# Kernel optimization log

Hardware: AMD Instinct MI355X
Metric: run time of the kernel (lower is better)

The kernel has to match this reference:

```python
import jax, jax.numpy as jnp
import numpy as np

TEMP = 5.0  # temperature_init
# All C(4,2)=6 keep-2-of-4 patterns for 2:4 semi-structured sparsity
PATTERNS = jnp.array([[1,1,0,0],[1,0,1,0],[1,0,0,1],[0,1,1,0],[0,1,0,1],[0,0,1,1]], dtype=jnp.float32)


def masked_linear(x, w, b, alpha, ids):
    # x: [N, I], w: [O, I], alpha: [A, O, I//4, 6], ids: [N]
    A, O, G, P = alpha.shape
    probs = jax.nn.softmax(alpha / TEMP, axis=-1)            # [A, O, G, 6]
    mask = jnp.einsum('aogp,pk->aogk', probs, PATTERNS)      # [A, O, G, 4]
    wm = w[None, :, :] * mask.reshape(A, O, G * 4)           # [A, O, I] per-agent masked weight
    y = jnp.einsum('ni,aoi->nao', x, wm)                     # dense per-agent GEMM
    y = jnp.take_along_axis(y, ids[:, None, None], axis=1)[:, 0, :]
    return y + b


def gru_cell(x, h, w_ih, w_hh, b_ih, b_hh):
    gi = x @ w_ih.T + b_ih
    gh = h @ w_hh.T + b_hh
    i_r, i_z, i_n = jnp.split(gi, 3, axis=-1)
    h_r, h_z, h_n = jnp.split(gh, 3, axis=-1)
    r = jax.nn.sigmoid(i_r + h_r)
    z = jax.nn.sigmoid(i_z + h_z)
    n = jnp.tanh(i_n + r * h_n)
    return (1.0 - z) * n + z * h


def setup_inputs() -> dict:
    key = jax.random.key(0)
    ks = jax.random.split(key, 20)
    B, A, E, H, NA = 1024, 8, 64, 512, 16
    s = 0.05
    d = {}
    d['inputs'] = jax.random.normal(ks[0], (B, A, E), jnp.float32)
    d['hidden_state'] = jax.random.normal(ks[1], (B, A, H), jnp.float32)
    d['agent_ids'] = jax.random.randint(ks[2], (B, A), 0, A, jnp.int32)
    d['fc1_w'] = jax.random.normal(ks[3], (H, E), jnp.float32) * s
    d['fc1_b'] = jax.random.normal(ks[4], (H,), jnp.float32) * s
    d['fc1_alpha'] = jax.random.normal(ks[5], (A, H, E // 4, 6), jnp.float32)
    d['gru_w_ih'] = jax.random.normal(ks[6], (3 * H, H), jnp.float32) * s
    d['gru_w_hh'] = jax.random.normal(ks[7], (3 * H, H), jnp.float32) * s
    d['gru_b_ih'] = jax.random.normal(ks[8], (3 * H,), jnp.float32) * s
    d['gru_b_hh'] = jax.random.normal(ks[9], (3 * H,), jnp.float32) * s
    d['fc2_w'] = jax.random.normal(ks[10], (H, H), jnp.float32) * s
    d['fc2_b'] = jax.random.normal(ks[11], (H,), jnp.float32) * s
    d['fc2_alpha'] = jax.random.normal(ks[12], (A, H, H // 4, 6), jnp.float32)
    d['fc3_w'] = jax.random.normal(ks[13], (H, H), jnp.float32) * s
    d['fc3_b'] = jax.random.normal(ks[14], (H,), jnp.float32) * s
    d['fc3_alpha'] = jax.random.normal(ks[15], (A, H, H // 4, 6), jnp.float32)
    d['fc4_w'] = jax.random.normal(ks[16], (NA, H), jnp.float32) * s
    d['fc4_b'] = jax.random.normal(ks[17], (NA,), jnp.float32) * s
    d['fc4_alpha'] = jax.random.normal(ks[18], (A, NA, H // 4, 6), jnp.float32)
    return d


def reference(inputs, hidden_state, agent_ids,
              fc1_w, fc1_b, fc1_alpha,
              gru_w_ih, gru_w_hh, gru_b_ih, gru_b_hh,
              fc2_w, fc2_b, fc2_alpha,
              fc3_w, fc3_b, fc3_alpha,
              fc4_w, fc4_b, fc4_alpha):
    b, a, e = inputs.shape
    H = hidden_state.shape[-1]
    x = inputs.reshape(-1, e)
    ids = agent_ids.reshape(-1)
    x = jax.nn.relu(masked_linear(x, fc1_w, fc1_b, fc1_alpha, ids))
    h = gru_cell(x, hidden_state.reshape(-1, H), gru_w_ih, gru_w_hh, gru_b_ih, gru_b_hh)
    q = jax.nn.relu(masked_linear(h, fc2_w, fc2_b, fc2_alpha, ids))
    q = jax.nn.relu(masked_linear(q, fc3_w, fc3_b, fc3_alpha, ids))
    q = masked_linear(q, fc4_w, fc4_b, fc4_alpha, ids)
    return q.reshape(b, a, -1), h.reshape(b, a, -1)
```

## Files before the change

kernel.cpp:

```cpp
#include <hip/hip_runtime.h>
#include <hip/hip_bf16.h>

typedef unsigned short ushort_t;
typedef __bf16 bf16x8 __attribute__((ext_vector_type(8)));
typedef unsigned short us8 __attribute__((ext_vector_type(8)));
typedef float f32x4 __attribute__((ext_vector_type(4)));

__device__ __forceinline__ ushort_t f2b(float f) {
    union { float f; unsigned int u; } v; v.f = f;
    unsigned int u = v.u;
    unsigned int r = (u + 0x7FFFu + ((u >> 16) & 1u)) >> 16;
    return (ushort_t)r;
}
__device__ __forceinline__ float sigmoidf_(float x) {
    return 1.f / (1.f + __expf(-x));
}
__device__ __forceinline__ void store_o(ushort_t* p, float v) { *p = f2b(v); }
__device__ __forceinline__ void store_o(float* p, float v) { *p = v; }

__global__ void fill_kernel(float* out, long long n, float val) {
    long long i = (long long)blockIdx.x * blockDim.x + threadIdx.x;
    if (i < n) out[i] = val;
}

#define PACKSZ(O, K) ((long long)((O) >= 64 ? (O) >> 6 : 1) * ((K) >> 5) * 2048)

__device__ __forceinline__ void maskw_item(const float* __restrict__ alpha,
                                           const float* __restrict__ w,
                                           ushort_t* __restrict__ wm,
                                           long long idx, int O, int G, int dup) {
    int g = (int)(idx % G);
    long long t2 = idx / G;
    int o = (int)(t2 % O);
    int a = (int)(t2 / O);
    const float* al = alpha + idx * 6;
    float p[6];
    float mx = -1e30f;
    #pragma unroll
    for (int i = 0; i < 6; i++) { p[i] = al[i] * 0.2f; mx = fmaxf(mx, p[i]); }
    float s = 0.f;
    #pragma unroll
    for (int i = 0; i < 6; i++) { p[i] = __expf(p[i] - mx); s += p[i]; }
    float inv = 1.f / s;
    #pragma unroll
    for (int i = 0; i < 6; i++) p[i] *= inv;
    float mk[4] = { p[0] + p[1] + p[2], p[0] + p[3] + p[4],
                    p[1] + p[3] + p[5], p[2] + p[4] + p[5] };
    int K = G * 4;
    const float* wr = w + (long long)o * K + g * 4;
    ushort_t* base = wm + (long long)a * PACKSZ(O, K);
    int k0 = g * 4;
    int c = o >> 6, su = (o >> 4) & 3, n = o & 15;
    int kk = k0 >> 5, q = (k0 >> 3) & 3, e0 = k0 & 7;
    long long off = (((long long)(c * (K >> 5) + kk) * 4 + su) * 64 + (q * 16 + n)) * 8 + e0;
    #pragma unroll
    for (int t = 0; t < 4; t++) {
        ushort_t v = f2b(wr[t] * mk[t]);
        base[off + t] = v;
        if (dup) {
            base[off + t + 512] = v;
            base[off + t + 1024] = v;
            base[off + t + 1536] = v;
        }
    }
}

__device__ __forceinline__ void canon_pack_item(const float* __restrict__ src,
                                                ushort_t* __restrict__ dst,
                                                long long i) {
    long long base = i * 8;
    int o_full = (int)(base >> 9);
    int k0 = (int)(base & 511);
    int g = o_full >> 9, o = o_full & 511;
    int c = o >> 6, su = (o >> 4) & 3, n = o & 15;
    int kk = k0 >> 5, q = (k0 >> 3) & 3;
    long long off = (long long)g * 262144 +
        (((long long)(c * 16 + kk) * 4 + su) * 64 + (q * 16 + n)) * 8;
    us8 v;
    #pragma unroll
    for (int e = 0; e < 8; e++) v[e] = f2b(src[base + e]);
    *(us8*)(dst + off) = v;
}

__device__ __forceinline__ void canon_gather_item(const float* __restrict__ src,
                                                  ushort_t* __restrict__ dst,
                                                  const int* __restrict__ perm,
                                                  int ld, long long i) {
    long long base = i * 8;
    int pos = (int)(base / ld);
    int k = (int)(base % ld);
    int row = perm[pos] & 8191;
    const float* s = src + (long long)row * ld + k;
    us8 v;
    #pragma unroll
    for (int e = 0; e < 8; e++) v[e] = f2b(s[e]);
    *(us8*)(dst + base) = v;
}

#define W_FC1 65536LL
#define W_FC2 589824LL
#define W_FC3 1114112LL
#define W_FC4 1130496LL
#define W_WIH 1228800LL
#define W_END 1327104LL
#define SPW_BLOCKS (1 + 1296)

__global__ void sort_prepw(const int* __restrict__ ids,
                           int* __restrict__ perm, int* __restrict__ seg,
                           int4* __restrict__ ttab, int* __restrict__ tcount,
                           const float* fc1_al, const float* fc1_w, ushort_t* wm1,
                           const float* fc2_al, const float* fc2_w, ushort_t* wm2,
                           const float* fc3_al, const float* fc3_w, ushort_t* wm3,
                           const float* fc4_al, const float* fc4_w, ushort_t* wm4,
                           const float* wih, ushort_t* wihp,
                           const float* whh, ushort_t* whhp) {
    int tid = threadIdx.x;
    if (blockIdx.x == 0) {
        __shared__ int hist[16][8];
        __shared__ int wbase[16][8];
        __shared__ int atot[8];
        __shared__ int abase[8];
        int wave = tid >> 6, lane = tid & 63;
        int base = wave * 512;
        unsigned long long lt = (lane == 63) ? 0x7fffffffffffffffull
                                             : ((1ull << lane) - 1ull);
        int myid[8], rank[8];
        int run[8] = {0, 0, 0, 0, 0, 0, 0, 0};
        #pragma unroll
        for (int i = 0; i < 8; i++) myid[i] = ids[base + i * 64 + lane] & 7;
        #pragma unroll
        for (int i = 0; i < 8; i++) {
            int a = myid[i];
            int r = 0;
            #pragma unroll
            for (int a2 = 0; a2 < 8; a2++) {
                unsigned long long m = __ballot(a == a2);
                if (a2 == a) r = run[a2] + __popcll(m & lt);
                run[a2] += __popcll(m);
            }
            rank[i] = r;
        }
        if (lane == 0) {
            #pragma unroll
            for (int a = 0; a < 8; a++) hist[wave][a] = run[a];
        }
        __syncthreads();
        if (tid < 8) {
            int a = tid, s = 0;
            for (int w = 0; w < 16; w++) { wbase[w][a] = s; s += hist[w][a]; }
            atot[a] = s;
        }
        __syncthreads();
        if (tid == 0) {
            int s = 0;
            for (int a = 0; a < 8; a++) { abase[a] = s; seg[a] = s; s += atot[a]; }
            seg[8] = s;
            int T = 0;
            for (int a = 0; a < 8; a++)
                for (int m = abase[a]; m < abase[a] + atot[a]; m += 64) {
                    int e = abase[a] + atot[a];
                    if (e > m + 64) e = m + 64;
                    ttab[T++] = make_int4(a, m, e, 0);
                }
            *tcount = T;
        }
        __syncthreads();
        #pragma unroll
        for (int i = 0; i < 8; i++) {
            int a = myid[i];
            perm[abase[a] + wbase[wave][a] + rank[i]] = base + i * 64 + lane;
        }
        return;
    }
    long long gid = (long long)(blockIdx.x - 1) * 1024 + tid;
    if (gid < W_FC1)      { maskw_item(fc1_al, fc1_w, wm1, gid, 512, 16, 0); return; }
    if (gid < W_FC2)      { maskw_item(fc2_al, fc2_w, wm2, gid - W_FC1, 512, 128, 0); return; }
    if (gid < W_FC3)      { maskw_item(fc3_al, fc3_w, wm3, gid - W_FC2, 512, 128, 0); return; }
    if (gid < W_FC4)      { maskw_item(fc4_al, fc4_w, wm4, gid - W_FC3, 16, 128, 1); return; }
    if (gid < W_WIH)      { canon_pack_item(wih, wihp, gid - W_FC4); return; }
    canon_pack_item(whh, whhp, gid - W_WIH);
}

#define G_INP 65536LL
#define G_END 589824LL
#define PG_BLOCKS 576

__global__ void prep_gather(const float* __restrict__ inputs, ushort_t* inp_pos,
                            const float* __restrict__ hidden, ushort_t* hid_pos,
                            const int* __restrict__ perm) {
    long long gid = (long long)blockIdx.x * 1024 + threadIdx.x;
    if (gid < G_INP) canon_gather_item(inputs, inp_pos, perm, 64, gid);
    else             canon_gather_item(hidden, hid_pos, perm, 512, gid - G_INP);
}

#define BM 64
#define BN 64

template <typename OT>
__launch_bounds__(256, 4)
__global__ void gemm_tiled(const ushort_t* __restrict__ In, int ldin,
                           const ushort_t* __restrict__ Wpk, long long wstride,
                           const float* __restrict__ bias,
                           OT* __restrict__ Out, int ldo,
                           const int4* __restrict__ ttab,
                           const int* __restrict__ tcount,
                           const int* __restrict__ scatter,
                           int O, int K, int relu) {
    int t = blockIdx.x;
    if (t >= *tcount) return;
    int4 tt = ttab[t];
    int a = tt.x, pos0 = tt.y, pos1 = tt.z;
    int o0 = blockIdx.y * BN;

    __shared__ ushort_t As[2][2048];

    int tid = threadIdx.x;
    int wave = tid >> 6, lane = tid & 63;
    int wr = (wave >> 1) & 1, wc = wave & 1;
    int quad = lane >> 4, l16 = lane & 15;
    int srow = tid >> 2, sgrp = tid & 3;
    int wsoff = (srow * 4 + (sgrp ^ ((srow >> 2) & 3))) * 8;
    int rl = (l16 * 4 + (quad ^ ((l16 >> 2) & 3))) * 8;

    int apos = pos0 + srow;
    int apos_c = apos < pos1 ? apos : (pos1 - 1);
    const ushort_t* aptr = In + (long long)apos_c * ldin + sgrp * 8;

    const ushort_t* wb = Wpk + (long long)a * wstride +
        (long long)blockIdx.y * (K >> 5) * 2048 + lane * 8;

    f32x4 acc[2][2];
    #pragma unroll
    for (int i = 0; i < 2; i++)
        #pragma unroll
        for (int j = 0; j < 2; j++) acc[i][j] = (f32x4){0.f, 0.f, 0.f, 0.f};

    int KKh = K >> 6;
    for (int k2 = 0; k2 < KKh; k2++) {
        int kk = k2 * 2;
        us8 av0 = *(const us8*)(aptr + kk * 32);
        us8 av1 = *(const us8*)(aptr + kk * 32 + 32);
        bf16x8 b00 = *(const bf16x8*)(wb + (kk * 4 + wc * 2 + 0) * 512);
        bf16x8 b01 = *(const bf16x8*)(wb + (kk * 4 + wc * 2 + 1) * 512);
        bf16x8 b10 = *(const bf16x8*)(wb + ((kk + 1) * 4 + wc * 2 + 0) * 512);
        bf16x8 b11 = *(const bf16x8*)(wb + ((kk + 1) * 4 + wc * 2 + 1) * 512);
        __syncthreads();
        *(us8*)(&As[0][wsoff]) = av0;
        *(us8*)(&As[1][wsoff]) = av1;
        __syncthreads();
        bf16x8 af0[2], af1[2];
        af0[0] = *(const bf16x8*)(&As[0][(wr * 2 + 0) * 512 + rl]);
        af0[1] = *(const bf16x8*)(&As[0][(wr * 2 + 1) * 512 + rl]);
        af1[0] = *(const bf16x8*)(&As[1][(wr * 2 + 0) * 512 + rl]);
        af1[1] = *(const bf16x8*)(&As[1][(wr * 2 + 1) * 512 + rl]);
        #pragma unroll
        for (int i = 0; i < 2; i++) {
            acc[i][0] = __builtin_amdgcn_mfma_f32_16x16x32_bf16(af0[i], b00, acc[i][0], 0, 0, 0);
            acc[i][1] = __builtin_amdgcn_mfma_f32_16x16x32_bf16(af0[i], b01, acc[i][1], 0, 0, 0);
        }
        #pragma unroll
        for (int i = 0; i < 2; i++) {
            acc[i][0] = __builtin_amdgcn_mfma_f32_16x16x32_bf16(af1[i], b10, acc[i][0], 0, 0, 0);
            acc[i][1] = __builtin_amdgcn_mfma_f32_16x16x32_bf16(af1[i], b11, acc[i][1], 0, 0, 0);
        }
    }

    #pragma unroll
    for (int i = 0; i < 2; i++) {
        int mbase = wr * 32 + i * 16 + quad * 4;
        #pragma unroll
        for (int j = 0; j < 2; j++) {
            int col = o0 + wc * 32 + j * 16 + l16;
            if (col < O) {
                float bias_v = bias ? bias[col] : 0.f;
                #pragma unroll
                for (int r = 0; r < 4; r++) {
                    int pos = pos0 + mbase + r;
                    if (pos < pos1) {
                        float v = acc[i][j][r] + bias_v;
                        if (relu) v = fmaxf(v, 0.f);
                        int orow = (scatter ? scatter[pos] : pos) & 8191;
                        store_o(&Out[(long long)orow * ldo + col], v);
                    }
                }
            }
        }
    }
}

__launch_bounds__(512, 2)
__global__ void gru_fused(const ushort_t* __restrict__ y1,
                          const ushort_t* __restrict__ hid_pos,
                          const float* __restrict__ hidden_f,
                          const ushort_t* __restrict__ wihp,
                          const ushort_t* __restrict__ whhp,
                          const float* __restrict__ bih,
                          const float* __restrict__ bhh,
                          const int* __restrict__ perm,
                          float* __restrict__ out_h_f,
                          ushort_t* __restrict__ hp,
                          int N, int H) {
    int m0 = blockIdx.x * 128;

    __shared__ ushort_t Ay[4096];
    __shared__ ushort_t Ah[4096];
    __shared__ ushort_t Bt[6][2048];

    int tid = threadIdx.x;
    int wave = tid >> 6, lane = tid & 63;
    int wr = wave >> 1, wc = wave & 1;
    int quad = lane >> 4, l16 = lane & 15;
    int srow = tid >> 2, sgrp = tid & 3;
    int wsoff = (srow * 4 + (sgrp ^ ((srow >> 2) & 3))) * 8;
    int rl = (l16 * 4 + (quad ^ ((l16 >> 2) & 3))) * 8;

    const ushort_t* ay_p = y1 + (long long)(m0 + srow) * H + sgrp * 8;
    const ushort_t* ah_p = hid_pos + (long long)(m0 + srow) * H + sgrp * 8;

    const ushort_t* wbs[3];
    int wg[3];
    #pragma unroll
    for (int q = 0; q < 3; q++) {
        int s = q * 512 + tid;
        int g = s >> 8, so = s & 255;
        wg[q] = s;
        wbs[q] = ((g < 3) ? (wihp + (long long)g * 262144)
                          : (whhp + (long long)(g - 3) * 262144)) +
                 (long long)blockIdx.y * 16 * 2048 + so * 8;
    }

    f32x4 acc[4][2][2];
    #pragma unroll
    for (int g = 0; g < 4; g++)
        #pragma unroll
        for (int i = 0; i < 2; i++)
            #pragma unroll
            for (int j = 0; j < 2; j++) acc[g][i][j] = (f32x4){0.f, 0.f, 0.f, 0.f};

    for (int kk = 0; kk < 16; kk++) {
        us8 va = *(const us8*)(ay_p + kk * 32);
        us8 vh = *(const us8*)(ah_p + kk * 32);
        us8 vb[3];
        #pragma unroll
        for (int q = 0; q < 3; q++) vb[q] = *(const us8*)(wbs[q] + kk * 2048);
        __syncthreads();
        *(us8*)(&Ay[wsoff]) = va;
        *(us8*)(&Ah[wsoff]) = vh;
        #pragma unroll
        for (int q = 0; q < 3; q++) {
            int s = wg[q];
            *(us8*)(&Bt[s >> 8][(s & 255) * 8]) = vb[q];
        }
        __syncthreads();

        bf16x8 ayf[2], ahf[2];
        #pragma unroll
        for (int u = 0; u < 2; u++) {
            ayf[u] = *(const bf16x8*)(&Ay[(wr * 2 + u) * 512 + rl]);
            ahf[u] = *(const bf16x8*)(&Ah[(wr * 2 + u) * 512 + rl]);
        }
        #pragma unroll
        for (int g = 0; g < 3; g++) {
            bf16x8 bw[2], bu[2];
            #pragma unroll
            for (int u = 0; u < 2; u++) {
                bw[u] = *(const bf16x8*)(&Bt[g][(wc * 2 + u) * 512 + lane * 8]);
                bu[u] = *(const bf16x8*)(&Bt[g + 3][(wc * 2 + u) * 512 + lane * 8]);
            }
            int ai = (g < 2) ? g : 2;
            int ah2 = (g < 2) ? g : 3;
            #pragma unroll
            for (int i = 0; i < 2; i++)
                #pragma unroll
                for (int j = 0; j < 2; j++) {
                    acc[ai][i][j] = __builtin_amdgcn_mfma_f32_16x16x32_bf16(
                        ayf[i], bw[j], acc[ai][i][j], 0, 0, 0);
                    acc[ah2][i][j] = __builtin_amdgcn_mfma_f32_16x16x32_bf16(
                        ahf[i], bu[j], acc[ah2][i][j], 0, 0, 0);
                }
        }
    }

    int c0 = blockIdx.y * 64;
    #pragma unroll
    for (int i = 0; i < 2; i++) {
        #pragma unroll
        for (int r = 0; r < 4; r++) {
            int pos = m0 + wr * 32 + i * 16 + quad * 4 + r;
            int norig = perm[pos] & 8191;
            #pragma unroll
            for (int j = 0; j < 2; j++) {
                int col = c0 + wc * 32 + j * 16 + l16;
                float sr = acc[0][i][j][r] + bih[col] + bhh[col];
                float sz = acc[1][i][j][r] + bih[H + col] + bhh[H + col];
                float in_ = acc[2][i][j][r] + bih[2 * H + col];
                float hn = acc[3][i][j][r] + bhh[2 * H + col];
                float rg = sigmoidf_(sr);
                float zg = sigmoidf_(sz);
                float ng = tanhf(in_ + rg * hn);
                float hv = hidden_f[(long long)norig * H + col];
                float hnew = (1.f - zg) * ng + zg * hv;
                out_h_f[(long long)norig * H + col] = hnew;
                hp[(long long)pos * H + col] = f2b(hnew);
            }
        }
    }
}

extern "C" void kernel_launch(void* const* d_in, const int* in_sizes, int n_in,
                              void* d_out, int out_size, void* d_ws, size_t ws_size,
                              hipStream_t stream) {
    (void)in_sizes; (void)n_in;
    const int N = 8192, A = 8, E = 64, H = 512, NA = 16;

    float* out_f = (float*)d_out;
    float* out_q = out_f;
    float* out_h = out_f + (size_t)N * NA;

    char* p = (char*)d_ws;
    auto alloc = [&](size_t b) { char* r = p; p += (b + 255) & ~(size_t)255; return r; };
    int*  perm   = (int*)alloc((size_t)N * 4);
    int*  seg    = (int*)alloc(16 * 4);
    int4* ttab   = (int4*)alloc(144 * 16);
    int*  tcount = (int*)alloc(256);
    ushort_t* wm1     = (ushort_t*)alloc((size_t)A * PACKSZ(H, E) * 2);
    ushort_t* wm2     = (ushort_t*)alloc((size_t)A * PACKSZ(H, H) * 2);
    ushort_t* wm3     = (ushort_t*)alloc((size_t)A * PACKSZ(H, H) * 2);
    ushort_t* wm4     = (ushort_t*)alloc((size_t)A * PACKSZ(NA, H) * 2);
    ushort_t* y1      = (ushort_t*)alloc((size_t)N * H * 2);
    ushort_t* inp_pos = (ushort_t*)alloc((size_t)N * E * 2);
    ushort_t* hid_pos = (ushort_t*)alloc((size_t)N * H * 2);
    ushort_t* wihp    = (ushort_t*)alloc((size_t)3 * H * H * 2);
    ushort_t* whhp    = (ushort_t*)alloc((size_t)3 * H * H * 2);
    ushort_t* hp      = (ushort_t*)alloc((size_t)N * H * 2);
    size_t need = (size_t)(p - (char*)d_ws);
    ushort_t* q2 = y1;
    ushort_t* q3 = hid_pos;

    if (ws_size < need) {
        fill_kernel<<<(unsigned)((out_size + 255) / 256), 256, 0, stream>>>(
            out_f, out_size, 1000.f);
        return;
    }

    const float* inputs = (const float*)d_in[0];
    const float* hidden = (const float*)d_in[1];
    const int*   ids    = (const int*)d_in[2];
    const float* fc1_w  = (const float*)d_in[3];
    const float* fc1_b  = (const float*)d_in[4];
    const float* fc1_al = (const float*)d_in[5];
    const float* wih    = (const float*)d_in[6];
    const float* whh    = (const float*)d_in[7];
    const float* bih    = (const float*)d_in[8];
    const float* bhh    = (const float*)d_in[9];
    const float* fc2_w  = (const float*)d_in[10];
    const float* fc2_b  = (const float*)d_in[11];
    const float* fc2_al = (const float*)d_in[12];
    const float* fc3_w  = (const float*)d_in[13];
    const float* fc3_b  = (const float*)d_in[14];
    const float* fc3_al = (const float*)d_in[15];
    const float* fc4_w  = (const float*)d_in[16];
    const float* fc4_b  = (const float*)d_in[17];
    const float* fc4_al = (const float*)d_in[18];

    sort_prepw<<<SPW_BLOCKS, 1024, 0, stream>>>(
        ids, perm, seg, ttab, tcount,
        fc1_al, fc1_w, wm1, fc2_al, fc2_w, wm2, fc3_al, fc3_w, wm3,
        fc4_al, fc4_w, wm4, wih, wihp, whh, whhp);

    prep_gather<<<PG_BLOCKS, 1024, 0, stream>>>(
        inputs, inp_pos, hidden, hid_pos, perm);

    dim3 blk(256);
    gemm_tiled<ushort_t><<<dim3(136, H / BN), blk, 0, stream>>>(
        inp_pos, E, wm1, PACKSZ(H, E), fc1_b, y1, H, ttab, tcount,
        nullptr, H, E, 1);
    gru_fused<<<dim3(N / 128, H / 64), dim3(512), 0, stream>>>(
        y1, hid_pos, hidden, wihp, whhp, bih, bhh, perm, out_h, hp, N, H);
    gemm_tiled<ushort_t><<<dim3(136, H / BN), blk, 0, stream>>>(
        hp, H, wm2, PACKSZ(H, H), fc2_b, q2, H, ttab, tcount,
        nullptr, H, H, 1);
    gemm_tiled<ushort_t><<<dim3(136, H / BN), blk, 0, stream>>>(
        q2, H, wm3, PACKSZ(H, H), fc3_b, q3, H, ttab, tcount,
        nullptr, H, H, 1);
    gemm_tiled<float><<<dim3(136, 1), blk, 0, stream>>>(
        q3, H, wm4, PACKSZ(NA, H), fc4_b, out_q, NA, ttab, tcount,
        perm, NA, H, 0);
}
```

Measured before the change: 214.0 us.

## Fuse input gather and hidden gather into a dedicated fc1 GEMM kernel

Replaces the separate prep_gather launch and the generic fc1 GEMM with a specialized gemm_fc1 kernel. It reads fp32 inputs directly through the permutation, converting to bf16 on the fly, so the inp_pos intermediate buffer is no longer needed. Extra blocks in the same grid perform the hidden-state gather for the GRU. This saves one launch and one round trip through global memory, but mixes two kinds of work in a single grid, and the fused K=64 path is fully unrolled with no pipelining.

```diff
diff --git a/kernel.cpp b/kernel.cpp
--- a/kernel.cpp
+++ b/kernel.cpp
@@ -181,16 +181,102 @@
     canon_pack_item(whh, whhp, gid - W_WIH);
 }
 
-#define G_INP 65536LL
-#define G_END 589824LL
-#define PG_BLOCKS 576
-
-__global__ void prep_gather(const float* __restrict__ inputs, ushort_t* inp_pos,
-                            const float* __restrict__ hidden, ushort_t* hid_pos,
-                            const int* __restrict__ perm) {
-    long long gid = (long long)blockIdx.x * 1024 + threadIdx.x;
-    if (gid < G_INP) canon_gather_item(inputs, inp_pos, perm, 64, gid);
-    else             canon_gather_item(hidden, hid_pos, perm, 512, gid - G_INP);
+__launch_bounds__(256, 4)
+__global__ void gemm_fc1(const float* __restrict__ inputs,
+                         const ushort_t* __restrict__ Wpk,
+                         long long wstride,
+                         const float* __restrict__ bias,
+                         ushort_t* __restrict__ Out, int ldo,
+                         const int4* __restrict__ ttab,
+                         const int* __restrict__ tcount,
+                         const int* __restrict__ perm,
+                         const float* __restrict__ hidden,
+                         ushort_t* __restrict__ hid_pos,
+                         int O) {
+    if (blockIdx.x >= 136) {
+        long long idx = ((long long)(blockIdx.x - 136) * 8 + blockIdx.y) * 256
+                        + threadIdx.x;
+        canon_gather_item(hidden, hid_pos, perm, 512, idx);
+        return;
+    }
+    int t = blockIdx.x;
+    if (t >= *tcount) return;
+    int4 tt = ttab[t];
+    int a = tt.x, pos0 = tt.y, pos1 = tt.z;
+    int o0 = blockIdx.y * 64;
+
+    __shared__ ushort_t As[2][2048];
+
+    int tid = threadIdx.x;
+    int wave = tid >> 6, lane = tid & 63;
+    int wr = (wave >> 1) & 1, wc = wave & 1;
+    int quad = lane >> 4, l16 = lane & 15;
+    int srow = tid >> 2, sgrp = tid & 3;
+    int wsoff = (srow * 4 + (sgrp ^ ((srow >> 2) & 3))) * 8;
+    int rl = (l16 * 4 + (quad ^ ((l16 >> 2) & 3))) * 8;
+
+    int apos = pos0 + srow;
+    int apos_c = apos < pos1 ? apos : (pos1 - 1);
+    int arow = perm[apos_c] & 8191;
+    const float* ap = inputs + (long long)arow * 64 + sgrp * 8;
+
+    const ushort_t* wb = Wpk + (long long)a * wstride +
+        (long long)blockIdx.y * 2 * 2048 + lane * 8;
+
+    f32x4 acc[2][2];
+    #pragma unroll
+    for (int i = 0; i < 2; i++)
+        #pragma unroll
+        for (int j = 0; j < 2; j++) acc[i][j] = (f32x4){0.f, 0.f, 0.f, 0.f};
+
+    us8 av0, av1;
+    #pragma unroll
+    for (int e = 0; e < 8; e++) {
+        av0[e] = f2b(ap[e]);
+        av1[e] = f2b(ap[32 + e]);
+    }
+    bf16x8 b00 = *(const bf16x8*)(wb + (0 * 4 + wc * 2 + 0) * 512);
+    bf16x8 b01 = *(const bf16x8*)(wb + (0 * 4 + wc * 2 + 1) * 512);
+    bf16x8 b10 = *(const bf16x8*)(wb + (1 * 4 + wc * 2 + 0) * 512);
+    bf16x8 b11 = *(const bf16x8*)(wb + (1 * 4 + wc * 2 + 1) * 512);
+    *(us8*)(&As[0][wsoff]) = av0;
+    *(us8*)(&As[1][wsoff]) = av1;
+    __syncthreads();
+    bf16x8 af0[2], af1[2];
+    af0[0] = *(const bf16x8*)(&As[0][(wr * 2 + 0) * 512 + rl]);
+    af0[1] = *(const bf16x8*)(&As[0][(wr * 2 + 1) * 512 + rl]);
+    af1[0] = *(const bf16x8*)(&As[1][(wr * 2 + 0) * 512 + rl]);
+    af1[1] = *(const bf16x8*)(&As[1][(wr * 2 + 1) * 512 + rl]);
+    #pragma unroll
+    for (int i = 0; i < 2; i++) {
+        acc[i][0] = __builtin_amdgcn_mfma_f32_16x16x32_bf16(af0[i], b00, acc[i][0], 0, 0, 0);
+        acc[i][1] = __builtin_amdgcn_mfma_f32_16x16x32_bf16(af0[i], b01, acc[i][1], 0, 0, 0);
+    }
+    #pragma unroll
+    for (int i = 0; i < 2; i++) {
+        acc[i][0] = __builtin_amdgcn_mfma_f32_16x16x32_bf16(af1[i], b10, acc[i][0], 0, 0, 0);
+        acc[i][1] = __builtin_amdgcn_mfma_f32_16x16x32_bf16(af1[i], b11, acc[i][1], 0, 0, 0);
+    }
+
+    #pragma unroll
+    for (int i = 0; i < 2; i++) {
+        int mbase = wr * 32 + i * 16 + quad * 4;
+        #pragma unroll
+        for (int j = 0; j < 2; j++) {
+            int col = o0 + wc * 32 + j * 16 + l16;
+            if (col < O) {
+                float bias_v = bias[col];
+                #pragma unroll
+                for (int r = 0; r < 4; r++) {
+                    int pos = pos0 + mbase + r;
+                    if (pos < pos1) {
+                        float v = fmaxf(acc[i][j][r] + bias_v, 0.f);
+                        Out[(long long)pos * ldo + col] = f2b(v);
+                    }
+                }
+            }
+        }
+    }
 }
 
 #define BM 64
@@ -428,7 +514,6 @@
     ushort_t* wm3     = (ushort_t*)alloc((size_t)A * PACKSZ(H, H) * 2);
     ushort_t* wm4     = (ushort_t*)alloc((size_t)A * PACKSZ(NA, H) * 2);
     ushort_t* y1      = (ushort_t*)alloc((size_t)N * H * 2);
-    ushort_t* inp_pos = (ushort_t*)alloc((size_t)N * E * 2);
     ushort_t* hid_pos = (ushort_t*)alloc((size_t)N * H * 2);
     ushort_t* wihp    = (ushort_t*)alloc((size_t)3 * H * H * 2);
     ushort_t* whhp    = (ushort_t*)alloc((size_t)3 * H * H * 2);
@@ -468,13 +553,10 @@
         fc1_al, fc1_w, wm1, fc2_al, fc2_w, wm2, fc3_al, fc3_w, wm3,
         fc4_al, fc4_w, wm4, wih, wihp, whh, whhp);
 
-    prep_gather<<<PG_BLOCKS, 1024, 0, stream>>>(
-        inputs, inp_pos, hidden, hid_pos, perm);
-
     dim3 blk(256);
-    gemm_tiled<ushort_t><<<dim3(136, H / BN), blk, 0, stream>>>(
-        inp_pos, E, wm1, PACKSZ(H, E), fc1_b, y1, H, ttab, tcount,
-        nullptr, H, E, 1);
+    gemm_fc1<<<dim3(136 + 256, 8), blk, 0, stream>>>(
+        inputs, wm1, PACKSZ(H, E), fc1_b, y1, H, ttab, tcount,
+        perm, hidden, hid_pos, H);
     gru_fused<<<dim3(N / 128, H / 64), dim3(512), 0, stream>>>(
         y1, hid_pos, hidden, wihp, whhp, bih, bhh, perm, out_h, hp, N, H);
     gemm_tiled<ushort_t><<<dim3(136, H / BN), blk, 0, stream>>>(
```

After: 208.8 us. -2.4%, faster.
